# Kernel tuning notes

Hardware: AMD Instinct MI355X
Metric: run time of the kernel (lower is better)

## Reference

```python
import jax, jax.numpy as jnp
import numpy as np
import math

IN_CH = 512
OUT_CH = 512
K = 3
STYLE_DIM = 512
EPS = 1e-8


def setup_inputs() -> dict:
    key = jax.random.key(0)
    k1, k2, k3, k4 = jax.random.split(key, 4)
    x = jax.random.normal(k1, (16, IN_CH, 64, 64), dtype=jnp.float32)
    style = jax.random.normal(k2, (16, STYLE_DIM), dtype=jnp.float32)
    weight = jax.random.normal(k3, (OUT_CH, IN_CH, K, K), dtype=jnp.float32)
    affine_w = jax.random.normal(k4, (IN_CH, STYLE_DIM), dtype=jnp.float32)
    affine_b = jnp.ones((IN_CH,), dtype=jnp.float32)  # bias_init=1.0
    return {"x": x, "style": style, "weight": weight,
            "affine_w": affine_w, "affine_b": affine_b}


def reference(x, style, weight, affine_w, affine_b):
    # EqualizedLinear: weight_scale = 1/sqrt(style_dim), lr_multiplier = 1
    w_scale = 1.0 / math.sqrt(STYLE_DIM)
    s = style @ (affine_w * w_scale).T + affine_b  # [B, Ci]

    # Demodulation factor: sigma_inv[b,o] = rsqrt(sum_{i,k,k} (w[o,i,k,k]*s[b,i])^2 + eps)
    wsq = jnp.sum(weight ** 2, axis=(2, 3))               # [Co, Ci]
    sigma_inv = jax.lax.rsqrt(jnp.einsum('oi,bi->bo', wsq, s ** 2) + EPS)  # [B, Co]

    # Modulated grouped conv == scale input per-channel, shared-weight conv,
    # scale output per-channel (conv is linear in the weight).
    x_mod = x * s[:, :, None, None]                        # [B, Ci, H, W]
    pad = K // 2
    y = jax.lax.conv_general_dilated(
        x_mod, weight,
        window_strides=(1, 1),
        padding=((pad, pad), (pad, pad)),
        dimension_numbers=('NCHW', 'OIHW', 'NCHW'))       # [B, Co, H, W]
    y = y * sigma_inv[:, :, None, None]
    return y
```

## Files before the change

### kernel.cpp

```cpp
#include <hip/hip_runtime.h>
#include <hip/hip_bf16.h>

#define BATCH 16
#define CI    512
#define CO    512
#define IMG   64
#define HP    66
#define NPIX  4096
#define NTAP  9

typedef __bf16  bf16x8  __attribute__((ext_vector_type(8)));
typedef float   floatx4 __attribute__((ext_vector_type(4)));

#define OFF_S     0u
#define OFF_SIG   32768u
#define OFF_WSQ   65536u
#define OFF_WBF   1114112u
#define OFF_XPAD  5832704u
#define XPAD_BYTES 71368704u
#define WS_NEEDED (OFF_XPAD + XPAD_BYTES)

__global__ void k_style(const float* __restrict__ style, const float* __restrict__ aw,
                        const float* __restrict__ ab, float* __restrict__ s_out)
{
    __shared__ float st[512];
    int b = blockIdx.x;
    int t = threadIdx.x;
    st[t]       = style[b * 512 + t];
    st[t + 256] = style[b * 512 + t + 256];
    __syncthreads();
    int i = blockIdx.y * 256 + t;
    const float4* awr = (const float4*)(aw + (size_t)i * 512);
    float sum = 0.f;
#pragma unroll 8
    for (int k = 0; k < 128; ++k) {
        float4 v = awr[k];
        sum += v.x * st[4 * k] + v.y * st[4 * k + 1] + v.z * st[4 * k + 2] + v.w * st[4 * k + 3];
    }
    s_out[b * 512 + i] = sum * 0.04419417382415922f + ab[i];
}

__global__ void k_wprep(const float* __restrict__ wgt, float* __restrict__ wsq,
                        unsigned short* __restrict__ wbf)
{
    int idx = blockIdx.x * 256 + threadIdx.x;
    const float* p = wgt + (size_t)idx * 9;
    float q = 0.f;
#pragma unroll
    for (int t9 = 0; t9 < 9; ++t9) {
        float v = p[t9];
        q += v * v;
        __hip_bfloat16 hv = __float2bfloat16(v);
        wbf[t9 * 262144 + idx] = *(unsigned short*)&hv;
    }
    wsq[idx] = q;
}

__global__ void k_sigma(const float* __restrict__ s_in, const float* __restrict__ wsq,
                        float* __restrict__ sig)
{
    __shared__ float s2[512];
    int b = blockIdx.x, t = threadIdx.x;
    float a0 = s_in[b * 512 + t], a1 = s_in[b * 512 + t + 256];
    s2[t] = a0 * a0;
    s2[t + 256] = a1 * a1;
    __syncthreads();
    int o = blockIdx.y * 256 + t;
    const float4* wr = (const float4*)(wsq + (size_t)o * 512);
    float sum = 0.f;
#pragma unroll 8
    for (int k = 0; k < 128; ++k) {
        float4 v = wr[k];
        sum += v.x * s2[4 * k] + v.y * s2[4 * k + 1] + v.z * s2[4 * k + 2] + v.w * s2[4 * k + 3];
    }
    sig[b * 512 + o] = rsqrtf(sum + 1e-8f);
}

__global__ void k_xmod(const float* __restrict__ x, const float* __restrict__ s_in,
                       unsigned short* __restrict__ xpad)
{
    __shared__ float tile[64][65];
    int b = blockIdx.x, h = blockIdx.y, cic = blockIdx.z;
    int t = threadIdx.x;
    int lane_w = t & 63, grp = t >> 6;
    int ci0 = cic * 64;
#pragma unroll 4
    for (int it = 0; it < 16; ++it) {
        int ci_l = grp * 16 + it;
        int ci = ci0 + ci_l;
        float v = x[(((size_t)(b * 512 + ci)) << 12) + (h << 6) + lane_w] * s_in[b * 512 + ci];
        tile[ci_l][lane_w] = v;
    }
    __syncthreads();
#pragma unroll 4
    for (int it = 0; it < 16; ++it) {
        int w_l = grp * 16 + it;
        float v = tile[lane_w][w_l];
        __hip_bfloat16 hv = __float2bfloat16(v);
        xpad[((size_t)((b * 66 + h + 1) * 66 + (w_l + 1))) * 512 + ci0 + lane_w] = *(unsigned short*)&hv;
    }
}

__device__ __forceinline__ void gload16(const void* g, void* l)
{
    __builtin_amdgcn_global_load_lds(
        (const __attribute__((address_space(1))) unsigned int*)g,
        (__attribute__((address_space(3))) unsigned int*)l, 16, 0, 0);
}

__global__ __launch_bounds__(256, 2)
void k_conv(const unsigned short* __restrict__ xpad, const unsigned short* __restrict__ wbf,
            const float* __restrict__ sig, float* __restrict__ y)
{
    __shared__ unsigned short A_lds[4096];
    __shared__ unsigned short B_lds[4096];
    int t = threadIdx.x;
    int w = t >> 6, l = t & 63;
    int wr = w >> 1, wc = w & 1;
    int bx = blockIdx.x;
    int b = bx >> 7, rem = bx & 127;
    int co_t = rem >> 5, pix_t = rem & 31;
    int o_base = co_t << 7;
    int h0 = pix_t << 1;

    const char* wb = (const char*)wbf;
    const char* xb = (const char*)xpad;

    int idx0 = (w << 6) + l;
    int idx1 = idx0 + 256;
    int aoff0 = ((o_base + (idx0 >> 2)) << 10) + ((idx0 & 3) << 4);
    int aoff1 = ((o_base + (idx1 >> 2)) << 10) + ((idx1 & 3) << 4);
    int p0 = idx0 >> 2, p1 = idx1 >> 2;
    int boff0 = (((b * 66 + h0 + (p0 >> 6)) * 66 + (p0 & 63)) << 10) + ((idx0 & 3) << 4);
    int boff1 = (((b * 66 + h0 + (p1 >> 6)) * 66 + (p1 & 63)) << 10) + ((idx1 & 3) << 4);
    char* aL0 = (char*)A_lds + (w << 10);
    char* aL1 = (char*)A_lds + 4096 + (w << 10);
    char* bL0 = (char*)B_lds + (w << 10);
    char* bL1 = (char*)B_lds + 4096 + (w << 10);

    floatx4 acc[4][4];
#pragma unroll
    for (int i = 0; i < 4; ++i)
#pragma unroll
        for (int j = 0; j < 4; ++j)
            acc[i][j] = (floatx4){0.f, 0.f, 0.f, 0.f};

    int fa = wr * 2048 + (l & 15) * 32 + (l >> 4) * 8;
    int fb = wc * 2048 + (l & 15) * 32 + (l >> 4) * 8;

    for (int tap = 0; tap < 9; ++tap) {
        int kh = tap / 3;
        int kw = tap - kh * 3;
        int tb = (kh * 66 + kw) << 10;
        int ta = tap << 19;
        for (int cic = 0; cic < 16; ++cic) {
            int kb = cic << 6;
            gload16(wb + ta + kb + aoff0, aL0);
            gload16(wb + ta + kb + aoff1, aL1);
            gload16(xb + tb + kb + boff0, bL0);
            gload16(xb + tb + kb + boff1, bL1);
            __syncthreads();

            bf16x8 af[4], bfr[4];
#pragma unroll
            for (int i = 0; i < 4; ++i) af[i]  = *(const bf16x8*)&A_lds[fa + i * 512];
#pragma unroll
            for (int j = 0; j < 4; ++j) bfr[j] = *(const bf16x8*)&B_lds[fb + j * 512];
#pragma unroll
            for (int i = 0; i < 4; ++i)
#pragma unroll
                for (int j = 0; j < 4; ++j)
                    acc[i][j] = __builtin_amdgcn_mfma_f32_16x16x32_bf16(af[i], bfr[j], acc[i][j], 0, 0, 0);
            __syncthreads();
        }
    }

    int col = l & 15, quad = l >> 4;
    const float* sb = sig + b * 512;
#pragma unroll
    for (int i = 0; i < 4; ++i) {
        int ob = o_base + wr * 64 + i * 16 + quad * 4;
#pragma unroll
        for (int r = 0; r < 4; ++r) {
            int o = ob + r;
            float sv = sb[o];
            float* yrow = y + (((size_t)(b * 512 + o)) << 12);
#pragma unroll
            for (int j = 0; j < 4; ++j) {
                int pix = (pix_t << 7) + wc * 64 + j * 16 + col;
                yrow[pix] = acc[i][j][r] * sv;
            }
        }
    }
}

extern "C" void kernel_launch(void* const* d_in, const int* in_sizes, int n_in,
                              void* d_out, int out_size, void* d_ws, size_t ws_size,
                              hipStream_t stream)
{
    const float* x        = (const float*)d_in[0];
    const float* style    = (const float*)d_in[1];
    const float* weight   = (const float*)d_in[2];
    const float* affine_w = (const float*)d_in[3];
    const float* affine_b = (const float*)d_in[4];
    float* y = (float*)d_out;

    if (ws_size < (size_t)WS_NEEDED) {
        return;
    }

    char* ws = (char*)d_ws;
    float*          s_buf = (float*)(ws + OFF_S);
    float*          sig   = (float*)(ws + OFF_SIG);
    float*          wsq   = (float*)(ws + OFF_WSQ);
    unsigned short* wbf   = (unsigned short*)(ws + OFF_WBF);
    unsigned short* xpad  = (unsigned short*)(ws + OFF_XPAD);

    hipMemsetAsync(xpad, 0, XPAD_BYTES, stream);
    k_style<<<dim3(16, 2), 256, 0, stream>>>(style, affine_w, affine_b, s_buf);
    k_wprep<<<1024, 256, 0, stream>>>(weight, wsq, wbf);
    k_sigma<<<dim3(16, 2), 256, 0, stream>>>(s_buf, wsq, sig);
    k_xmod<<<dim3(16, 64, 8), 256, 0, stream>>>(x, s_buf, xpad);
    k_conv<<<2048, 256, 0, stream>>>(xpad, wbf, sig, y);
}
```

Measured before the change: 622.0 us.

## Zero only halo, vectorize xmod transpose, swizzle conv LDS layout

```diff
diff --git a/kernel.cpp b/kernel.cpp
--- a/kernel.cpp
+++ b/kernel.cpp
@@ -76,28 +76,60 @@
     sig[b * 512 + o] = rsqrtf(sum + 1e-8f);
 }
 
+__global__ void k_halo(unsigned short* __restrict__ xpad)
+{
+    int b = blockIdx.x, p = blockIdx.y, t = threadIdx.x;
+    int h, w;
+    if (p < 66)       { h = 0;            w = p; }
+    else if (p < 132) { h = 65;           w = p - 66; }
+    else if (p < 196) { h = 1 + (p - 132); w = 0; }
+    else              { h = 1 + (p - 196); w = 65; }
+    unsigned int* dst = (unsigned int*)(xpad + ((size_t)((b * 66 + h) * 66 + w)) * 512);
+    dst[t] = 0u;
+}
+
 __global__ void k_xmod(const float* __restrict__ x, const float* __restrict__ s_in,
                        unsigned short* __restrict__ xpad)
 {
-    __shared__ float tile[64][65];
-    int b = blockIdx.x, h = blockIdx.y, cic = blockIdx.z;
+    __shared__ unsigned short tile[64 * 256];
+    __shared__ float sm_s[256];
+    int b = blockIdx.x, h = blockIdx.y, half = blockIdx.z;
+    int ci0 = half * 256;
     int t = threadIdx.x;
-    int lane_w = t & 63, grp = t >> 6;
-    int ci0 = cic * 64;
-#pragma unroll 4
-    for (int it = 0; it < 16; ++it) {
-        int ci_l = grp * 16 + it;
-        int ci = ci0 + ci_l;
-        float v = x[(((size_t)(b * 512 + ci)) << 12) + (h << 6) + lane_w] * s_in[b * 512 + ci];
-        tile[ci_l][lane_w] = v;
-    }
-    __syncthreads();
-#pragma unroll 4
-    for (int it = 0; it < 16; ++it) {
-        int w_l = grp * 16 + it;
-        float v = tile[lane_w][w_l];
-        __hip_bfloat16 hv = __float2bfloat16(v);
-        xpad[((size_t)((b * 66 + h + 1) * 66 + (w_l + 1))) * 512 + ci0 + lane_w] = *(unsigned short*)&hv;
+
+    sm_s[t] = s_in[b * 512 + ci0 + t];
+    __syncthreads();
+
+    int w0 = (t & 15) * 4;
+    int cp = (t >> 4) * 2;
+#pragma unroll
+    for (int i = 0; i < 8; ++i) {
+        int ci_l = i * 32 + cp;
+        float sv0 = sm_s[ci_l], sv1 = sm_s[ci_l + 1];
+        const float4 v0 = *(const float4*)(x + (((size_t)(b * 512 + ci0 + ci_l)) << 12) + (h << 6) + w0);
+        const float4 v1 = *(const float4*)(x + (((size_t)(b * 512 + ci0 + ci_l + 1)) << 12) + (h << 6) + w0);
+        float a0[4] = {v0.x, v0.y, v0.z, v0.w};
+        float a1[4] = {v1.x, v1.y, v1.z, v1.w};
+#pragma unroll
+        for (int j = 0; j < 4; ++j) {
+            int w = w0 + j;
+            __hip_bfloat16 h0 = __float2bfloat16(a0[j] * sv0);
+            __hip_bfloat16 h1 = __float2bfloat16(a1[j] * sv1);
+            unsigned int packed = (unsigned int)(*(unsigned short*)&h0)
+                                | ((unsigned int)(*(unsigned short*)&h1) << 16);
+            int off = w * 256 + (((ci_l >> 3) ^ ((w >> 2) & 7)) << 3) + (ci_l & 7);
+            *(unsigned int*)&tile[off] = packed;
+        }
+    }
+    __syncthreads();
+
+    int q = t & 31;
+#pragma unroll
+    for (int i = 0; i < 8; ++i) {
+        int w = i * 8 + (t >> 5);
+        int off = w * 256 + ((q ^ ((w >> 2) & 7)) << 3);
+        uint4 v = *(const uint4*)&tile[off];
+        *(uint4*)(xpad + ((size_t)((b * 66 + h + 1) * 66 + (w + 1))) * 512 + ci0 + q * 8) = v;
     }
 }
 
@@ -128,11 +160,12 @@
 
     int idx0 = (w << 6) + l;
     int idx1 = idx0 + 256;
-    int aoff0 = ((o_base + (idx0 >> 2)) << 10) + ((idx0 & 3) << 4);
-    int aoff1 = ((o_base + (idx1 >> 2)) << 10) + ((idx1 & 3) << 4);
+    int sw = (((idx0 & 3) ^ ((idx0 >> 3) & 3)) << 4);
+    int aoff0 = ((o_base + (idx0 >> 2)) << 10) + sw;
+    int aoff1 = ((o_base + (idx1 >> 2)) << 10) + sw;
     int p0 = idx0 >> 2, p1 = idx1 >> 2;
-    int boff0 = (((b * 66 + h0 + (p0 >> 6)) * 66 + (p0 & 63)) << 10) + ((idx0 & 3) << 4);
-    int boff1 = (((b * 66 + h0 + (p1 >> 6)) * 66 + (p1 & 63)) << 10) + ((idx1 & 3) << 4);
+    int boff0 = (((b * 66 + h0 + (p0 >> 6)) * 66 + (p0 & 63)) << 10) + sw;
+    int boff1 = (((b * 66 + h0 + (p1 >> 6)) * 66 + (p1 & 63)) << 10) + sw;
     char* aL0 = (char*)A_lds + (w << 10);
     char* aL1 = (char*)A_lds + 4096 + (w << 10);
     char* bL0 = (char*)B_lds + (w << 10);
@@ -145,8 +178,10 @@
         for (int j = 0; j < 4; ++j)
             acc[i][j] = (floatx4){0.f, 0.f, 0.f, 0.f};
 
-    int fa = wr * 2048 + (l & 15) * 32 + (l >> 4) * 8;
-    int fb = wc * 2048 + (l & 15) * 32 + (l >> 4) * 8;
+    int lr = l & 15;
+    int fsw = (((l >> 4) ^ ((lr >> 1) & 3)) << 3);
+    int fa = wr * 2048 + lr * 32 + fsw;
+    int fb = wc * 2048 + lr * 32 + fsw;
 
     for (int tap = 0; tap < 9; ++tap) {
         int kh = tap / 3;
@@ -205,9 +240,7 @@
     const float* affine_b = (const float*)d_in[4];
     float* y = (float*)d_out;
 
-    if (ws_size < (size_t)WS_NEEDED) {
-        return;
-    }
+    if (ws_size < (size_t)WS_NEEDED) return;
 
     char* ws = (char*)d_ws;
     float*          s_buf = (float*)(ws + OFF_S);
@@ -216,10 +249,10 @@
     unsigned short* wbf   = (unsigned short*)(ws + OFF_WBF);
     unsigned short* xpad  = (unsigned short*)(ws + OFF_XPAD);
 
-    hipMemsetAsync(xpad, 0, XPAD_BYTES, stream);
+    k_halo<<<dim3(16, 260), 256, 0, stream>>>(xpad);
     k_style<<<dim3(16, 2), 256, 0, stream>>>(style, affine_w, affine_b, s_buf);
     k_wprep<<<1024, 256, 0, stream>>>(weight, wsq, wbf);
     k_sigma<<<dim3(16, 2), 256, 0, stream>>>(s_buf, wsq, sig);
-    k_xmod<<<dim3(16, 64, 8), 256, 0, stream>>>(x, s_buf, xpad);
+    k_xmod<<<dim3(16, 64, 2), 256, 0, stream>>>(x, s_buf, xpad);
     k_conv<<<2048, 256, 0, stream>>>(xpad, wbf, sig, y);
 }
```

Result: slower. 639.7 us (+2.8%).
